# Kernel tuning notes

Measured on AMD Instinct MI355X. Metric: run time of the kernel, lower is better.

The kernel has to match this reference:

```python
import jax, jax.numpy as jnp
import numpy as np


def setup_inputs() -> dict:
    A, F, C = 9, 128, 20          # anchors per cell, feature map size, num classes
    B, L = 32, 64                 # batch, num GT labels
    N = A * F * F                 # total anchors
    rng = np.random.default_rng(0)
    # label_data rows: (class, cx, cy, w, h); boxes strictly positive for log()
    lcls = rng.integers(0, C, L)
    lbox = rng.uniform(8.0, 100.0, (L, 4))
    label_data = np.concatenate([lcls[:, None].astype(np.float64), lbox], axis=1).astype(np.float32)
    # occurrence index of each label within its class (matches the inner count loop)
    occ = np.array([int(np.sum(lcls[:l] == lcls[l])) for l in range(L)])
    # anchor_data rows: (id, class, cx, cy, w, h, occurrence)
    a = np.zeros((N, 7), np.float32)
    a[:, 0] = np.arange(N)
    a[:, 1] = C  # background by default
    a[:, 2:6] = rng.uniform(8.0, 100.0, (N, 4))
    pos_idx = rng.choice(N, 128, replace=False)
    lab_pick = rng.integers(0, L, 128)
    a[pos_idx, 1] = lcls[lab_pick]
    a[pos_idx, 6] = occ[lab_pick]
    ign = rng.choice(np.setdiff1d(np.arange(N), pos_idx), 256, replace=False)
    a[ign, 1] = -1.0  # ignored anchors
    # deterministic stand-in for random.sample(range(N), 300) per batch element
    neg_samples = np.stack([rng.choice(N, 300, replace=False) for _ in range(B)]).astype(np.int32)
    k1, k2 = jax.random.split(jax.random.key(0))
    return {
        "cla_map": jax.random.normal(k1, (B, 2 * A, F, F), jnp.float32),
        "reg_map": jax.random.normal(k2, (B, 4 * A, F, F), jnp.float32),
        "label_data": jnp.asarray(label_data),
        "anchor_data": jnp.asarray(a),
        "neg_samples": jnp.asarray(neg_samples),
        "num_anchors": A,
        "fmap_size": F,
        "num_classes": C,
    }


def _smooth_l1(d):
    ad = jnp.abs(d)
    return jnp.where(ad < 1.0, 0.5 * d * d, ad - 0.5)


def reference(cla_map, reg_map, label_data, anchor_data, neg_samples, num_anchors, fmap_size, num_classes):
    A, F, C = num_anchors, fmap_size, num_classes
    B = cla_map.shape[0]
    N = anchor_data.shape[0]
    L = label_data.shape[0]

    a_lbl = anchor_data[:, 1]
    a_box = anchor_data[:, 2:6]          # cx, cy, w, h
    a_occ = anchor_data[:, 6]
    pos_mask = (a_lbl != -1.0) & (a_lbl != C)   # [N]

    # per-label occurrence index within its class (replaces inner label loop)
    l_cls = label_data[:, 0]
    li = jnp.arange(L)
    occ = jnp.sum((l_cls[None, :] == l_cls[:, None]) & (li[None, :] < li[:, None]), axis=1)  # [L]
    match = (l_cls[None, :] == a_lbl[:, None]) & (occ[None, :].astype(a_occ.dtype) == a_occ[:, None])  # [N,L]
    gt_idx = jnp.argmax(match, axis=1)
    g = label_data[gt_idx]               # [N,5]

    t = jnp.stack([
        (g[:, 1] - a_box[:, 0]) / a_box[:, 2],
        (g[:, 2] - a_box[:, 1]) / a_box[:, 3],
        jnp.log(g[:, 3] / a_box[:, 2]),
        jnp.log(g[:, 4] / a_box[:, 3]),
    ], axis=1)                           # [N,4]

    # anchor -> (channel, h, w) mapping, exactly as in the torch loops
    i = jnp.arange(N)
    h = (i // A) % F
    w = (i // A) // F
    c4 = (i % A) * 4
    c2 = (i % A) * 2

    p_reg = reg_map[:, c4[:, None] + jnp.arange(4)[None, :], h[:, None], w[:, None]]  # [B,N,4]
    p_cls = cla_map[:, c2[:, None] + jnp.arange(2)[None, :], h[:, None], w[:, None]]  # [B,N,2]

    loss_reg = jnp.mean(_smooth_l1(p_reg - t[None]), axis=-1)            # [B,N] SmoothL1 mean over 4
    loss_cls_pos = -jax.nn.log_softmax(p_cls, axis=-1)[..., 1]           # CE with soft target [0,1]
    pos_loss = jnp.sum(jnp.where(pos_mask[None, :], loss_cls_pos + 4.0 * loss_reg, 0.0))
    P = jnp.sum(pos_mask)                # positive count (same for every batch element)

    # negatives: walk sampled indices, take background anchors until count >= 3*P
    is_neg = a_lbl[neg_samples] == C                     # [B,300]
    cum = jnp.cumsum(is_neg.astype(jnp.int32), axis=1)
    include = is_neg & (cum <= 3 * P)                    # [B,300]
    nh, nw, nc2 = h[neg_samples], w[neg_samples], c2[neg_samples]
    npc = cla_map[jnp.arange(B)[:, None, None],
                  nc2[:, :, None] + jnp.arange(2)[None, None, :],
                  nh[:, :, None], nw[:, :, None]]        # [B,300,2]
    neg_loss = -jax.nn.log_softmax(npc, axis=-1)[..., 0] # CE with soft target [1,0]
    neg_total = jnp.sum(jnp.where(include, neg_loss, 0.0))
    neg_count = jnp.sum(include)

    denom = (B * P + neg_count).astype(cla_map.dtype)
    return ((pos_loss + neg_total) / denom).reshape(1)
```

## Files before the change

kernel.cpp:

```cpp
#include <hip/hip_runtime.h>
#include <math.h>


#define MAXL 1024

__global__ void k_pos_scan(const float* __restrict__ anchor,
                           const float* __restrict__ label,
                           const float* __restrict__ cla,
                           const float* __restrict__ reg,
                           const int* __restrict__ dA,
                           const int* __restrict__ dF,
                           const int* __restrict__ dC,
                           int N, int L, int B,
                           int* __restrict__ cnt,
                           double* __restrict__ pos_loss) {
    const int A = *dA;
    const int F = *dF;
    const float Cf = (float)(*dC);

    __shared__ float sh_cls[MAXL];
    __shared__ int sh_occ[MAXL];
    const bool useLds = (L <= MAXL);
    if (useLds) {
        for (int j = threadIdx.x; j < L; j += blockDim.x)
            sh_cls[j] = label[(size_t)j * 5];
        __syncthreads();
        for (int j = threadIdx.x; j < L; j += blockDim.x) {
            float c = sh_cls[j];
            int o = 0;
            for (int k = 0; k < j; ++k) o += (sh_cls[k] == c) ? 1 : 0;
            sh_occ[j] = o;
        }
        __syncthreads();
    }

    int n = blockIdx.x * blockDim.x + threadIdx.x;
    if (n >= N) return;

    const float* a = anchor + (size_t)n * 7;
    float albl = a[1];
    if (albl == -1.0f || albl == Cf) return;

    atomicAdd(cnt, 1);

    float ax = a[2], ay = a[3], aw = a[4], ah = a[5], aocc = a[6];

    int gt = 0;
    for (int j = 0; j < L; ++j) {
        float cj;
        int oj;
        if (useLds) { cj = sh_cls[j]; oj = sh_occ[j]; }
        else {
            cj = label[(size_t)j * 5];
            oj = 0;
            for (int k = 0; k < j; ++k) oj += (label[(size_t)k * 5] == cj) ? 1 : 0;
        }
        if (cj == albl && (float)oj == aocc) { gt = j; break; }
    }
    const float* g = label + (size_t)gt * 5;
    float t0 = (g[1] - ax) / aw;
    float t1 = (g[2] - ay) / ah;
    float t2 = logf(g[3] / aw);
    float t3 = logf(g[4] / ah);

    int tmp = n / A;
    int ai  = n - tmp * A;
    int h   = tmp % F;
    int w   = tmp / F;
    int c4  = ai * 4;
    int c2  = ai * 2;
    size_t hw = (size_t)F * F;

    double acc = 0.0;
    for (int b = 0; b < B; ++b) {
        size_t regBase = (((size_t)b * (4 * A) + c4) * F + h) * F + w;
        float r0 = reg[regBase];
        float r1 = reg[regBase + hw];
        float r2 = reg[regBase + 2 * hw];
        float r3 = reg[regBase + 3 * hw];
        float d0 = r0 - t0, d1 = r1 - t1, d2 = r2 - t2, d3 = r3 - t3;

        float ad, sl, lr = 0.0f;
        ad = fabsf(d0); sl = (ad < 1.0f) ? 0.5f * d0 * d0 : ad - 0.5f; lr += sl;
        ad = fabsf(d1); sl = (ad < 1.0f) ? 0.5f * d1 * d1 : ad - 0.5f; lr += sl;
        ad = fabsf(d2); sl = (ad < 1.0f) ? 0.5f * d2 * d2 : ad - 0.5f; lr += sl;
        ad = fabsf(d3); sl = (ad < 1.0f) ? 0.5f * d3 * d3 : ad - 0.5f; lr += sl;
        lr *= 0.25f;

        size_t claBase = (((size_t)b * (2 * A) + c2) * F + h) * F + w;
        float x0 = cla[claBase];
        float x1 = cla[claBase + hw];
        float m = fmaxf(x0, x1);
        float lse = m + logf(expf(x0 - m) + expf(x1 - m));
        float lcp = lse - x1;

        acc += (double)(lcp + 4.0f * lr);
    }
    atomicAdd(pos_loss, acc);
}

__global__ void k_neg(const float* __restrict__ cla,
                      const float* __restrict__ anchor,
                      const int* __restrict__ neg,
                      const int* __restrict__ dA,
                      const int* __restrict__ dF,
                      const int* __restrict__ dC,
                      int S,
                      const int* __restrict__ cnt,
                      double* __restrict__ neg_loss,
                      int* __restrict__ neg_cnt) {
    const int A = *dA;
    const int F = *dF;
    const float Cf = (float)(*dC);
    const int P = *cnt;
    const int limit = 3 * P;

    int b = blockIdx.x;
    int lane = threadIdx.x;
    size_t hw = (size_t)F * F;

    int base = 0;
    float lsum = 0.0f;
    int lcnt = 0;

    for (int c0 = 0; c0 < S; c0 += 64) {
        int s = c0 + lane;
        bool valid = s < S;
        int idx = valid ? neg[(size_t)b * S + s] : 0;
        float lbl = valid ? anchor[(size_t)idx * 7 + 1] : -2.0f;
        bool isneg = valid && (lbl == Cf);

        unsigned long long mask = __ballot(isneg);
        int pre = __popcll(mask & ((1ull << lane) - 1ull));
        int cum = base + pre + (isneg ? 1 : 0);

        if (isneg && cum <= limit) {
            int tmp = idx / A;
            int ai  = idx - tmp * A;
            int h   = tmp % F;
            int w   = tmp / F;
            int c2  = ai * 2;
            size_t claBase = (((size_t)b * (2 * A) + c2) * F + h) * F + w;
            float x0 = cla[claBase];
            float x1 = cla[claBase + hw];
            float m = fmaxf(x0, x1);
            float lse = m + logf(expf(x0 - m) + expf(x1 - m));
            lsum += (lse - x0);
            lcnt += 1;
        }
        base += __popcll(mask);
    }

    for (int off = 32; off > 0; off >>= 1) {
        lsum += __shfl_down(lsum, off, 64);
        lcnt += __shfl_down(lcnt, off, 64);
    }
    if (lane == 0) {
        if (lsum != 0.0f) atomicAdd(neg_loss, (double)lsum);
        if (lcnt != 0) atomicAdd(neg_cnt, lcnt);
    }
}

__global__ void k_final(const int* __restrict__ cnt,
                        const int* __restrict__ neg_cnt,
                        const double* __restrict__ pos_loss,
                        const double* __restrict__ neg_loss,
                        int B,
                        float* __restrict__ out) {
    float denom = (float)(B * (*cnt) + (*neg_cnt));
    out[0] = (float)(*pos_loss + *neg_loss) / denom;
}

extern "C" void kernel_launch(void* const* d_in, const int* in_sizes, int n_in,
                              void* d_out, int out_size, void* d_ws, size_t ws_size,
                              hipStream_t stream) {
    const float* cla    = (const float*)d_in[0];
    const float* reg    = (const float*)d_in[1];
    const float* label  = (const float*)d_in[2];
    const float* anchor = (const float*)d_in[3];
    const int*   neg    = (const int*)d_in[4];
    const int*   dA     = (const int*)d_in[5];
    const int*   dF     = (const int*)d_in[6];
    const int*   dC     = (const int*)d_in[7];

    int N = in_sizes[3] / 7;
    int L = in_sizes[2] / 5;
    int B = in_sizes[0] / (2 * N);
    int S = in_sizes[4] / B;

    char* ws = (char*)d_ws;
    int*    cnt      = (int*)(ws + 0);
    int*    neg_cnt  = (int*)(ws + 4);
    double* pos_loss = (double*)(ws + 16);
    double* neg_loss = (double*)(ws + 24);

    hipMemsetAsync(ws, 0, 64, stream);

    int blk = 256;
    int grid = (N + blk - 1) / blk;
    k_pos_scan<<<grid, blk, 0, stream>>>(anchor, label, cla, reg, dA, dF, dC,
                                         N, L, B, cnt, pos_loss);
    k_neg<<<B, 64, 0, stream>>>(cla, anchor, neg, dA, dF, dC, S,
                                cnt, neg_loss, neg_cnt);
    k_final<<<1, 1, 0, stream>>>(cnt, neg_cnt, pos_loss, neg_loss, B,
                                 (float*)d_out);
}
```

Before: 169.6 us.

## Compact positive anchors, then spread per-batch loss work across threads

The scan kernel now only finds positive anchors and writes compact records (targets and spatial position) to workspace through an atomic slot counter, using a fixed 128-block grid-stride loop. A second kernel spreads the positive (anchor, batch) pairs across 16 blocks with wave-level double reductions, and handles negative sampling with one wave per batch in the remaining blocks, merging the former separate negative kernel. This removes the serial 32-iteration batch loop per positive thread and the per-thread double atomics. The cost is an extra workspace round trip and a dependency on the workspace holding every record; the LDS label cache is shrunk to 256 entries.

Result: faster. 157.1 us (-7.3%).

```diff
diff --git a/kernel.cpp b/kernel.cpp
--- a/kernel.cpp
+++ b/kernel.cpp
@@ -1,25 +1,29 @@
 #include <hip/hip_runtime.h>
 #include <math.h>
 
-
-#define MAXL 1024
-
-__global__ void k_pos_scan(const float* __restrict__ anchor,
-                           const float* __restrict__ label,
-                           const float* __restrict__ cla,
-                           const float* __restrict__ reg,
-                           const int* __restrict__ dA,
-                           const int* __restrict__ dF,
-                           const int* __restrict__ dC,
-                           int N, int L, int B,
-                           int* __restrict__ cnt,
-                           double* __restrict__ pos_loss) {
+#define MAXL 256
+
+struct __align__(16) PosRec {
+    float t0, t1, t2, t3;
+    int c2, h, w, pad;
+};
+
+__global__ void __launch_bounds__(256)
+k_scan(const float* __restrict__ anchor,
+       const float* __restrict__ label,
+       const int* __restrict__ dA,
+       const int* __restrict__ dF,
+       const int* __restrict__ dC,
+       int N, int L, int maxRec,
+       int* __restrict__ cnt,
+       PosRec* __restrict__ recs)
+{
     const int A = *dA;
     const int F = *dF;
     const float Cf = (float)(*dC);
 
     __shared__ float sh_cls[MAXL];
-    __shared__ int sh_occ[MAXL];
+    __shared__ int   sh_occ[MAXL];
     const bool useLds = (L <= MAXL);
     if (useLds) {
         for (int j = threadIdx.x; j < L; j += blockDim.x)
@@ -34,130 +38,151 @@
         __syncthreads();
     }
 
-    int n = blockIdx.x * blockDim.x + threadIdx.x;
-    if (n >= N) return;
-
-    const float* a = anchor + (size_t)n * 7;
-    float albl = a[1];
-    if (albl == -1.0f || albl == Cf) return;
-
-    atomicAdd(cnt, 1);
-
-    float ax = a[2], ay = a[3], aw = a[4], ah = a[5], aocc = a[6];
-
-    int gt = 0;
-    for (int j = 0; j < L; ++j) {
-        float cj;
-        int oj;
-        if (useLds) { cj = sh_cls[j]; oj = sh_occ[j]; }
-        else {
-            cj = label[(size_t)j * 5];
-            oj = 0;
-            for (int k = 0; k < j; ++k) oj += (label[(size_t)k * 5] == cj) ? 1 : 0;
-        }
-        if (cj == albl && (float)oj == aocc) { gt = j; break; }
+    const int tid = blockIdx.x * blockDim.x + threadIdx.x;
+    const int nth = gridDim.x * blockDim.x;
+
+    for (int n = tid; n < N; n += nth) {
+        float albl = anchor[(size_t)n * 7 + 1];
+        if (albl == -1.0f || albl == Cf) continue;
+
+        float ax   = anchor[(size_t)n * 7 + 2];
+        float ay   = anchor[(size_t)n * 7 + 3];
+        float aw   = anchor[(size_t)n * 7 + 4];
+        float ah   = anchor[(size_t)n * 7 + 5];
+        float aocc = anchor[(size_t)n * 7 + 6];
+
+        int gt = 0;
+        for (int j = 0; j < L; ++j) {
+            float cj; int oj;
+            if (useLds) { cj = sh_cls[j]; oj = sh_occ[j]; }
+            else {
+                cj = label[(size_t)j * 5];
+                oj = 0;
+                for (int k = 0; k < j; ++k) oj += (label[(size_t)k * 5] == cj) ? 1 : 0;
+            }
+            if (cj == albl && (float)oj == aocc) { gt = j; break; }
+        }
+        const float* g = label + (size_t)gt * 5;
+
+        PosRec r;
+        r.t0 = (g[1] - ax) / aw;
+        r.t1 = (g[2] - ay) / ah;
+        r.t2 = logf(g[3] / aw);
+        r.t3 = logf(g[4] / ah);
+        int tmp = n / A;
+        int ai  = n - tmp * A;
+        r.h = tmp % F;
+        r.w = tmp / F;
+        r.c2 = ai * 2;
+        r.pad = 0;
+
+        int slot = atomicAdd(cnt, 1);
+        if (slot < maxRec) recs[slot] = r;
     }
-    const float* g = label + (size_t)gt * 5;
-    float t0 = (g[1] - ax) / aw;
-    float t1 = (g[2] - ay) / ah;
-    float t2 = logf(g[3] / aw);
-    float t3 = logf(g[4] / ah);
-
-    int tmp = n / A;
-    int ai  = n - tmp * A;
-    int h   = tmp % F;
-    int w   = tmp / F;
-    int c4  = ai * 4;
-    int c2  = ai * 2;
-    size_t hw = (size_t)F * F;
-
-    double acc = 0.0;
-    for (int b = 0; b < B; ++b) {
-        size_t regBase = (((size_t)b * (4 * A) + c4) * F + h) * F + w;
-        float r0 = reg[regBase];
-        float r1 = reg[regBase + hw];
-        float r2 = reg[regBase + 2 * hw];
-        float r3 = reg[regBase + 3 * hw];
-        float d0 = r0 - t0, d1 = r1 - t1, d2 = r2 - t2, d3 = r3 - t3;
-
-        float ad, sl, lr = 0.0f;
-        ad = fabsf(d0); sl = (ad < 1.0f) ? 0.5f * d0 * d0 : ad - 0.5f; lr += sl;
-        ad = fabsf(d1); sl = (ad < 1.0f) ? 0.5f * d1 * d1 : ad - 0.5f; lr += sl;
-        ad = fabsf(d2); sl = (ad < 1.0f) ? 0.5f * d2 * d2 : ad - 0.5f; lr += sl;
-        ad = fabsf(d3); sl = (ad < 1.0f) ? 0.5f * d3 * d3 : ad - 0.5f; lr += sl;
-        lr *= 0.25f;
-
-        size_t claBase = (((size_t)b * (2 * A) + c2) * F + h) * F + w;
-        float x0 = cla[claBase];
-        float x1 = cla[claBase + hw];
-        float m = fmaxf(x0, x1);
-        float lse = m + logf(expf(x0 - m) + expf(x1 - m));
-        float lcp = lse - x1;
-
-        acc += (double)(lcp + 4.0f * lr);
-    }
-    atomicAdd(pos_loss, acc);
-}
-
-__global__ void k_neg(const float* __restrict__ cla,
-                      const float* __restrict__ anchor,
-                      const int* __restrict__ neg,
-                      const int* __restrict__ dA,
-                      const int* __restrict__ dF,
-                      const int* __restrict__ dC,
-                      int S,
-                      const int* __restrict__ cnt,
-                      double* __restrict__ neg_loss,
-                      int* __restrict__ neg_cnt) {
+}
+
+#define POS_BLOCKS 16
+#define NEG_BLOCKS 8
+
+__global__ void __launch_bounds__(256)
+k_loss(const float* __restrict__ cla,
+       const float* __restrict__ reg,
+       const float* __restrict__ anchor,
+       const int* __restrict__ neg,
+       const int* __restrict__ dA,
+       const int* __restrict__ dF,
+       const int* __restrict__ dC,
+       int B, int S,
+       const int* __restrict__ cnt,
+       const PosRec* __restrict__ recs,
+       double* __restrict__ pos_loss,
+       double* __restrict__ neg_loss,
+       int* __restrict__ neg_cnt)
+{
     const int A = *dA;
     const int F = *dF;
-    const float Cf = (float)(*dC);
+    const size_t hw = (size_t)F * F;
     const int P = *cnt;
-    const int limit = 3 * P;
-
-    int b = blockIdx.x;
-    int lane = threadIdx.x;
-    size_t hw = (size_t)F * F;
-
-    int base = 0;
-    float lsum = 0.0f;
-    int lcnt = 0;
-
-    for (int c0 = 0; c0 < S; c0 += 64) {
-        int s = c0 + lane;
-        bool valid = s < S;
-        int idx = valid ? neg[(size_t)b * S + s] : 0;
-        float lbl = valid ? anchor[(size_t)idx * 7 + 1] : -2.0f;
-        bool isneg = valid && (lbl == Cf);
-
-        unsigned long long mask = __ballot(isneg);
-        int pre = __popcll(mask & ((1ull << lane) - 1ull));
-        int cum = base + pre + (isneg ? 1 : 0);
-
-        if (isneg && cum <= limit) {
-            int tmp = idx / A;
-            int ai  = idx - tmp * A;
-            int h   = tmp % F;
-            int w   = tmp / F;
-            int c2  = ai * 2;
-            size_t claBase = (((size_t)b * (2 * A) + c2) * F + h) * F + w;
+    const int lane = threadIdx.x & 63;
+
+    if (blockIdx.x < POS_BLOCKS) {
+        const int tid = blockIdx.x * blockDim.x + threadIdx.x;
+        const int nth = POS_BLOCKS * blockDim.x;
+        const int T = P * B;
+
+        double acc = 0.0;
+        for (int task = tid; task < T; task += nth) {
+            int p = task / B;
+            int b = task - p * B;
+            PosRec r = recs[p];
+            int c4 = r.c2 * 2;
+
+            size_t regBase = (((size_t)b * (4 * A) + c4) * F + r.h) * F + r.w;
+            float d0 = reg[regBase]          - r.t0;
+            float d1 = reg[regBase +     hw] - r.t1;
+            float d2 = reg[regBase + 2 * hw] - r.t2;
+            float d3 = reg[regBase + 3 * hw] - r.t3;
+
+            float lr = 0.0f, ad;
+            ad = fabsf(d0); lr += (ad < 1.0f) ? 0.5f * d0 * d0 : ad - 0.5f;
+            ad = fabsf(d1); lr += (ad < 1.0f) ? 0.5f * d1 * d1 : ad - 0.5f;
+            ad = fabsf(d2); lr += (ad < 1.0f) ? 0.5f * d2 * d2 : ad - 0.5f;
+            ad = fabsf(d3); lr += (ad < 1.0f) ? 0.5f * d3 * d3 : ad - 0.5f;
+            lr *= 0.25f;
+
+            size_t claBase = (((size_t)b * (2 * A) + r.c2) * F + r.h) * F + r.w;
             float x0 = cla[claBase];
             float x1 = cla[claBase + hw];
-            float m = fmaxf(x0, x1);
+            float m  = fmaxf(x0, x1);
             float lse = m + logf(expf(x0 - m) + expf(x1 - m));
-            lsum += (lse - x0);
-            lcnt += 1;
-        }
-        base += __popcll(mask);
-    }
-
-    for (int off = 32; off > 0; off >>= 1) {
-        lsum += __shfl_down(lsum, off, 64);
-        lcnt += __shfl_down(lcnt, off, 64);
-    }
-    if (lane == 0) {
-        if (lsum != 0.0f) atomicAdd(neg_loss, (double)lsum);
-        if (lcnt != 0) atomicAdd(neg_cnt, lcnt);
+
+            acc += (double)((lse - x1) + 4.0f * lr);
+        }
+        for (int off = 32; off > 0; off >>= 1) acc += __shfl_down(acc, off, 64);
+        if (lane == 0 && acc != 0.0) atomicAdd(pos_loss, acc);
+    } else {
+        const float Cf = (float)(*dC);
+        int gwave = (blockIdx.x - POS_BLOCKS) * (blockDim.x >> 6) + (threadIdx.x >> 6);
+        if (gwave >= B) return;
+        int b = gwave;
+        const int limit = 3 * P;
+
+        int base = 0;
+        float lsum = 0.0f;
+        int lcnt = 0;
+        for (int c0 = 0; c0 < S; c0 += 64) {
+            int s = c0 + lane;
+            bool valid = (s < S);
+            int idx   = valid ? neg[(size_t)b * S + s] : 0;
+            float lbl = valid ? anchor[(size_t)idx * 7 + 1] : -2.0f;
+            bool isneg = valid && (lbl == Cf);
+
+            unsigned long long mask = __ballot(isneg);
+            int pre = __popcll(mask & ((1ull << lane) - 1ull));
+            int cum = base + pre + (isneg ? 1 : 0);
+
+            if (isneg && cum <= limit) {
+                int tmp = idx / A;
+                int ai  = idx - tmp * A;
+                int h   = tmp % F;
+                int w2  = tmp / F;
+                size_t claBase = (((size_t)b * (2 * A) + ai * 2) * F + h) * F + w2;
+                float x0 = cla[claBase];
+                float x1 = cla[claBase + hw];
+                float m  = fmaxf(x0, x1);
+                lsum += m + logf(expf(x0 - m) + expf(x1 - m)) - x0;
+                lcnt += 1;
+            }
+            base += __popcll(mask);
+        }
+        for (int off = 32; off > 0; off >>= 1) {
+            lsum += __shfl_down(lsum, off, 64);
+            lcnt += __shfl_down(lcnt, off, 64);
+        }
+        if (lane == 0 && lcnt != 0) {
+            atomicAdd(neg_loss, (double)lsum);
+            atomicAdd(neg_cnt, lcnt);
+        }
     }
 }
 
@@ -166,9 +191,10 @@
                         const double* __restrict__ pos_loss,
                         const double* __restrict__ neg_loss,
                         int B,
-                        float* __restrict__ out) {
-    float denom = (float)(B * (*cnt) + (*neg_cnt));
-    out[0] = (float)(*pos_loss + *neg_loss) / denom;
+                        float* __restrict__ out)
+{
+    double denom = (double)(B * (*cnt) + (*neg_cnt));
+    out[0] = (float)((*pos_loss + *neg_loss) / denom);
 }
 
 extern "C" void kernel_launch(void* const* d_in, const int* in_sizes, int n_in,
@@ -193,15 +219,21 @@
     int*    neg_cnt  = (int*)(ws + 4);
     double* pos_loss = (double*)(ws + 16);
     double* neg_loss = (double*)(ws + 24);
+    PosRec* recs     = (PosRec*)(ws + 64);
+    int maxRec = (int)((ws_size - 64) / sizeof(PosRec));
 
     hipMemsetAsync(ws, 0, 64, stream);
 
-    int blk = 256;
-    int grid = (N + blk - 1) / blk;
-    k_pos_scan<<<grid, blk, 0, stream>>>(anchor, label, cla, reg, dA, dF, dC,
-                                         N, L, B, cnt, pos_loss);
-    k_neg<<<B, 64, 0, stream>>>(cla, anchor, neg, dA, dF, dC, S,
-                                cnt, neg_loss, neg_cnt);
+    int scanGrid = 128;
+    k_scan<<<scanGrid, 256, 0, stream>>>(anchor, label, dA, dF, dC,
+                                         N, L, maxRec, cnt, recs);
+
+    int negBlocks = (B + 3) / 4;
+    int lossGrid = POS_BLOCKS + (negBlocks > NEG_BLOCKS ? negBlocks : NEG_BLOCKS);
+    k_loss<<<lossGrid, 256, 0, stream>>>(cla, reg, anchor, neg, dA, dF, dC,
+                                         B, S, cnt, recs,
+                                         pos_loss, neg_loss, neg_cnt);
+
     k_final<<<1, 1, 0, stream>>>(cnt, neg_cnt, pos_loss, neg_loss, B,
                                  (float*)d_out);
 }
```
